# Performance work log

Measured on AMD Instinct MI355X. Metric: run time of the kernel, lower is better.

The kernel has to match this reference:

```python
import jax, jax.numpy as jnp
import numpy as np

B, C, F, T = 8, 2, 64, 1024
E = C * F            # embed_dim = 128
H = 8                # num_heads
DH = E // H          # head_dim = 16


def setup_inputs() -> dict:
    key = jax.random.key(0)
    ks = jax.random.split(key, 14)
    s = 0.05  # small init scale for numerical stability
    return {
        "x_re": jax.random.normal(ks[0], (B, C, F, T), jnp.float32),
        "x_im": jax.random.normal(ks[1], (B, C, F, T), jnp.float32),
        "win_re": jax.random.normal(ks[2], (3 * E, E), jnp.float32) * s,
        "win_im": jax.random.normal(ks[3], (3 * E, E), jnp.float32) * s,
        "bin_re": jax.random.normal(ks[4], (3 * E,), jnp.float32) * s,
        "bin_im": jax.random.normal(ks[5], (3 * E,), jnp.float32) * s,
        "wout_re": jax.random.normal(ks[6], (E, E), jnp.float32) * s,
        "wout_im": jax.random.normal(ks[7], (E, E), jnp.float32) * s,
        "bout_re": jax.random.normal(ks[8], (E,), jnp.float32) * s,
        "bout_im": jax.random.normal(ks[9], (E,), jnp.float32) * s,
        "wt_re": jax.random.normal(ks[10], (E, E), jnp.float32) * s,
        "wt_im": jax.random.normal(ks[11], (E, E), jnp.float32) * s,
        "bt_re": jax.random.normal(ks[12], (E,), jnp.float32) * s,
        "bt_im": jax.random.normal(ks[13], (E,), jnp.float32) * s,
    }


def _forward(x_re, x_im, win_re, win_im, bin_re, bin_im,
             wout_re, wout_im, bout_re, bout_im,
             wt_re, wt_im, bt_re, bt_im):
    cplx = lambda r, i: (r + 1j * i).astype(jnp.complex64)
    x = cplx(x_re, x_im)                 # [B,C,F,T]
    win, bin_ = cplx(win_re, win_im), cplx(bin_re, bin_im)
    wout, bout = cplx(wout_re, wout_im), cplx(bout_re, bout_im)
    wt, bt = cplx(wt_re, wt_im), cplx(bt_re, bt_im)

    # flatten(1,2).transpose(1,2): [B,C,F,T] -> [B,E,T] -> [B,T,E]
    xs = jnp.transpose(x.reshape(B, E, T), (0, 2, 1))

    # packed complex qkv projection
    qkv = xs @ win.T + bin_              # [B,T,3E]
    q, k, v = jnp.split(qkv, 3, axis=-1)
    split_heads = lambda t: jnp.transpose(t.reshape(B, T, H, DH), (0, 2, 1, 3))
    q, k, v = split_heads(q), split_heads(k), split_heads(v)  # [B,H,T,DH]

    # complex attention scores Q K^H; softmax over real part
    scores = jnp.einsum("bhqd,bhkd->bhqk", q, jnp.conj(k)) * (DH ** -0.5)
    attn = jax.nn.softmax(scores.real, axis=-1).astype(jnp.complex64)
    o = jnp.einsum("bhqk,bhkd->bhqd", attn, v)               # [B,H,T,DH]
    o = jnp.transpose(o, (0, 2, 1, 3)).reshape(B, T, E)
    o = o @ wout.T + bout                # attention out-proj

    # transform: complex Linear E -> E
    y = o @ wt.T + bt                    # [B,T,E]

    # unflatten(-1,(C,F)) then movedim(1,-1): [B,T,C,F] -> [B,C,F,T]
    y = jnp.moveaxis(y.reshape(B, T, C, F), 1, -1)
    return jnp.stack([y.real, y.imag], axis=0)  # [2,B,C,F,T]


def reference(x_re, x_im, win_re, win_im, bin_re, bin_im,
              wout_re, wout_im, bout_re, bout_im,
              wt_re, wt_im, bt_re, bt_im):
    return _forward(x_re, x_im, win_re, win_im, bin_re, bin_im,
                    wout_re, wout_im, bout_re, bout_im,
                    wt_re, wt_im, bt_re, bt_im)
```

## Files before the change

kernel.cpp:

```cpp
#include <hip/hip_runtime.h>
#include <hip/hip_bf16.h>

#define B 8
#define T 1024
#define E 128
#define H 8
#define DH 16
#define E3 384

typedef __attribute__((ext_vector_type(8))) short short8;
typedef __attribute__((ext_vector_type(4))) short short4s;
typedef __attribute__((ext_vector_type(4))) float f32x4;

static __device__ inline short bf16s(float x) {
    union { float f; unsigned u; } v; v.f = x;
    unsigned r = v.u + 0x7fffu + ((v.u >> 16) & 1u);
    return (short)(r >> 16);
}

#if __has_builtin(__builtin_amdgcn_exp2f)
static __device__ inline float fexp2(float x) { return __builtin_amdgcn_exp2f(x); }
#else
static __device__ inline float fexp2(float x) { return __builtin_exp2f(x); }
#endif

static __device__ inline __hip_bfloat162 pk2(float a, float b) {
    float2 t; t.x = a; t.y = b;
    return __float22bfloat162_rn(t);
}

#define QSCALE 0.36067376022224085f

__global__ void prep_weights_kernel(
    const float* __restrict__ win_re, const float* __restrict__ win_im,
    const float* __restrict__ wout_re, const float* __restrict__ wout_im,
    const float* __restrict__ bout_re, const float* __restrict__ bout_im,
    const float* __restrict__ wt_re,   const float* __restrict__ wt_im,
    const float* __restrict__ bt_re,   const float* __restrict__ bt_im,
    short* __restrict__ Wp_re, short* __restrict__ Wp_im,
    short* __restrict__ Wfp_re, short* __restrict__ Wfp_im,
    float* __restrict__ bf_re, float* __restrict__ bf_im)
{
    int bid = blockIdx.x;
    if (bid < E3*E/256) {
        int idx = bid * 256 + threadIdx.x;
        int j = idx >> 7, e = idx & 127;
        float wr = win_re[idx], wi = win_im[idx];
        Wp_re[j*256 + e]       = bf16s(wr);
        Wp_re[j*256 + 128 + e] = bf16s(-wi);
        Wp_im[j*256 + e]       = bf16s(wi);
        Wp_im[j*256 + 128 + e] = bf16s(wr);
    } else {
        int idx = (bid - E3*E/256) * 256 + threadIdx.x;
        int j = idx >> 7, e = idx & 127;
        float ar = 0.f, ai = 0.f;
        for (int m = 0; m < E; ++m) {
            float tr = wt_re[j*E+m], ti = wt_im[j*E+m];
            float pr = wout_re[m*E+e], pi = wout_im[m*E+e];
            ar += tr*pr - ti*pi;
            ai += tr*pi + ti*pr;
        }
        Wfp_re[j*256 + e]       = bf16s(ar);
        Wfp_re[j*256 + 128 + e] = bf16s(-ai);
        Wfp_im[j*256 + e]       = bf16s(ai);
        Wfp_im[j*256 + 128 + e] = bf16s(ar);
        if (idx < E) {
            float br = bt_re[idx], bi = bt_im[idx];
            for (int m = 0; m < E; ++m) {
                float tr = wt_re[idx*E+m], ti = wt_im[idx*E+m];
                br += tr*bout_re[m] - ti*bout_im[m];
                bi += tr*bout_im[m] + ti*bout_re[m];
            }
            bf_re[idx] = br; bf_im[idx] = bi;
        }
    }
}

__global__ __launch_bounds__(256) void qkv_mfma_kernel(
    const float* __restrict__ x_re, const float* __restrict__ x_im,
    const short* __restrict__ Wp_re, const short* __restrict__ Wp_im,
    const float* __restrict__ bin_re, const float* __restrict__ bin_im,
    short* __restrict__ Qpk, short* __restrict__ Kpk,
    short* __restrict__ Vtre, short* __restrict__ Vtim)
{
    int tid  = threadIdx.x;
    int wave = tid >> 6, lane = tid & 63;
    int col  = lane & 15, quad = lane >> 4;
    int ttile = blockIdx.x;
    int b  = ttile >> 6;
    int tb = (ttile & 63) * 16 + col;

    short8 xf[8];
    #pragma unroll
    for (int kt = 0; kt < 8; ++kt) {
        const float* xs = (kt < 4) ? x_re : x_im;
        const float* p = &xs[((long)(b*E + (kt & 3)*32 + quad*8))*T + tb];
        float v0 = p[0], v1 = p[(long)T], v2 = p[2L*T], v3 = p[3L*T];
        float v4 = p[4L*T], v5 = p[5L*T], v6 = p[6L*T], v7 = p[7L*T];
        __hip_bfloat162* xp = (__hip_bfloat162*)&xf[kt];
        xp[0] = pk2(v0, v1); xp[1] = pk2(v2, v3);
        xp[2] = pk2(v4, v5); xp[3] = pk2(v6, v7);
    }

    const f32x4 zero = {0.f,0.f,0.f,0.f};

    #pragma unroll
    for (int half = 0; half < 2; ++half) {
        const short* Wsel = half ? Wp_im : Wp_re;
        const float* bias = half ? bin_im : bin_re;

        for (int ni = 0; ni < 6; ++ni) {
            int jt = wave * 6 + ni;
            const short* wrow = &Wsel[(jt*16 + col)*256 + quad*8];
            f32x4 acc = zero;
            #pragma unroll
            for (int kt = 0; kt < 8; ++kt) {
                short8 af = *(const short8*)(wrow + kt*32);
                acc = __builtin_amdgcn_mfma_f32_16x16x32_bf16(af, xf[kt], acc, 0, 0, 0);
            }
            int which = jt >> 3;
            int h = jt & 7;
            float scale = (which == 0) ? QSCALE : 1.0f;
            f32x4 res;
            #pragma unroll
            for (int r = 0; r < 4; ++r) {
                int jg = which*128 + h*16 + quad*4 + r;
                res[r] = (acc[r] + bias[jg]) * scale;
            }
            long bh = b*H + h;
            if (which == 2) {
                short* vt = half ? Vtim : Vtre;
                int tloc = tb & 31, tblk = tb & ~31;
                int u  = tloc & 15;
                int kk = (u >> 2)*8 + (u & 3) + ((tloc >= 16) ? 4 : 0);
                #pragma unroll
                for (int r = 0; r < 4; ++r)
                    vt[(bh*DH + quad*4 + r)*T + tblk + kk] = bf16s(res[r]);
            } else {
                short* qk = (which == 0) ? Qpk : Kpk;
                short4s pk;
                __hip_bfloat162* pp = (__hip_bfloat162*)&pk;
                pp[0] = pk2(res[0], res[1]);
                pp[1] = pk2(res[2], res[3]);
                *(short4s*)&qk[(bh*T + tb)*32 + half*16 + quad*4] = pk;
            }
        }
    }
}

__global__ __launch_bounds__(256) void attn_mfma_kernel(
    const short* __restrict__ Qpk, const short* __restrict__ Kpk,
    const short* __restrict__ Vtre, const short* __restrict__ Vtim,
    short* __restrict__ Opk)
{
    int id   = blockIdx.x;
    int bh   = id & 63;
    int q0   = (id >> 6) * 128;
    int tid  = threadIdx.x;
    int wave = tid >> 6;
    int lane = tid & 63;
    int col  = lane & 15;
    int quad = lane >> 4;

    long kq_base = (long)bh * T * 32;
    int qbase = q0 + wave * 32;

    short8 qfA = *(const short8*)&Qpk[kq_base + (long)(qbase + col)*32 + quad*8];
    short8 qfB = *(const short8*)&Qpk[kq_base + (long)(qbase + 16 + col)*32 + quad*8];

    const short* kp  = &Kpk[kq_base + col*32 + quad*8];
    const short* vrp = &Vtre[(long)bh*DH*T + (long)col*T + quad*8];
    const short* vip = &Vtim[(long)bh*DH*T + (long)col*T + quad*8];

    short8 ones;
    #pragma unroll
    for (int i = 0; i < 8; ++i) ones[i] = (short)0x3F80;

    f32x4 oAr = {0,0,0,0}, oAi = {0,0,0,0}, lA = {0,0,0,0};
    f32x4 oBr = {0,0,0,0}, oBi = {0,0,0,0}, lB = {0,0,0,0};
    const f32x4 zero = {0.f,0.f,0.f,0.f};

    auto STEP = [&](short8 kf0, short8 kf1, short8 vr, short8 vi) {
        __builtin_amdgcn_s_setprio(1);
        f32x4 sA0 = __builtin_amdgcn_mfma_f32_16x16x32_bf16(kf0, qfA, zero, 0, 0, 0);
        f32x4 sA1 = __builtin_amdgcn_mfma_f32_16x16x32_bf16(kf1, qfA, zero, 0, 0, 0);
        f32x4 sB0 = __builtin_amdgcn_mfma_f32_16x16x32_bf16(kf0, qfB, zero, 0, 0, 0);
        f32x4 sB1 = __builtin_amdgcn_mfma_f32_16x16x32_bf16(kf1, qfB, zero, 0, 0, 0);
        __builtin_amdgcn_s_setprio(0);

        short8 pfA, pfB;
        {
            __hip_bfloat162* pa = (__hip_bfloat162*)&pfA;
            pa[0] = pk2(fexp2(sA0[0]), fexp2(sA0[1]));
            pa[1] = pk2(fexp2(sA0[2]), fexp2(sA0[3]));
            pa[2] = pk2(fexp2(sA1[0]), fexp2(sA1[1]));
            pa[3] = pk2(fexp2(sA1[2]), fexp2(sA1[3]));
            __hip_bfloat162* pb = (__hip_bfloat162*)&pfB;
            pb[0] = pk2(fexp2(sB0[0]), fexp2(sB0[1]));
            pb[1] = pk2(fexp2(sB0[2]), fexp2(sB0[3]));
            pb[2] = pk2(fexp2(sB1[0]), fexp2(sB1[1]));
            pb[3] = pk2(fexp2(sB1[2]), fexp2(sB1[3]));
        }

        __builtin_amdgcn_s_setprio(1);
        oAr = __builtin_amdgcn_mfma_f32_16x16x32_bf16(vr, pfA, oAr, 0, 0, 0);
        oAi = __builtin_amdgcn_mfma_f32_16x16x32_bf16(vi, pfA, oAi, 0, 0, 0);
        lA  = __builtin_amdgcn_mfma_f32_16x16x32_bf16(ones, pfA, lA, 0, 0, 0);
        oBr = __builtin_amdgcn_mfma_f32_16x16x32_bf16(vr, pfB, oBr, 0, 0, 0);
        oBi = __builtin_amdgcn_mfma_f32_16x16x32_bf16(vi, pfB, oBi, 0, 0, 0);
        lB  = __builtin_amdgcn_mfma_f32_16x16x32_bf16(ones, pfB, lB, 0, 0, 0);
        __builtin_amdgcn_s_setprio(0);
    };

    short8 k0A = *(const short8*)kp;
    short8 k1A = *(const short8*)(kp + 512);
    short8 vrA = *(const short8*)vrp;
    short8 viA = *(const short8*)vip;
    short8 k0B = *(const short8*)(kp + 1024);
    short8 k1B = *(const short8*)(kp + 1536);
    short8 vrB = *(const short8*)(vrp + 32);
    short8 viB = *(const short8*)(vip + 32);
    kp += 2048; vrp += 64; vip += 64;

    for (int i = 0; i < 32; i += 2) {
        short8 k0n = *(const short8*)kp;
        short8 k1n = *(const short8*)(kp + 512);
        short8 vrn = *(const short8*)vrp;
        short8 vin = *(const short8*)vip;
        kp += 1024; vrp += 32; vip += 32;

        STEP(k0A, k1A, vrA, viA);
        k0A = k0n; k1A = k1n; vrA = vrn; viA = vin;

        k0n = *(const short8*)kp;
        k1n = *(const short8*)(kp + 512);
        vrn = *(const short8*)vrp;
        vin = *(const short8*)vip;
        kp += 1024; vrp += 32; vip += 32;

        STEP(k0B, k1B, vrB, viB);
        k0B = k0n; k1B = k1n; vrB = vrn; viB = vin;
    }

    int b = bh >> 3, h = bh & 7;
    float invA = 1.0f / lA[0];
    float invB = 1.0f / lB[0];

    long orowA = ((long)(b*T + qbase + col))*256 + h*16 + quad*4;
    {
        short4s pr, pi_;
        __hip_bfloat162* a = (__hip_bfloat162*)&pr;
        a[0] = pk2(oAr[0]*invA, oAr[1]*invA);
        a[1] = pk2(oAr[2]*invA, oAr[3]*invA);
        __hip_bfloat162* c = (__hip_bfloat162*)&pi_;
        c[0] = pk2(oAi[0]*invA, oAi[1]*invA);
        c[1] = pk2(oAi[2]*invA, oAi[3]*invA);
        *(short4s*)&Opk[orowA]       = pr;
        *(short4s*)&Opk[orowA + 128] = pi_;
    }
    long orowB = orowA + 16L*256;
    {
        short4s pr, pi_;
        __hip_bfloat162* a = (__hip_bfloat162*)&pr;
        a[0] = pk2(oBr[0]*invB, oBr[1]*invB);
        a[1] = pk2(oBr[2]*invB, oBr[3]*invB);
        __hip_bfloat162* c = (__hip_bfloat162*)&pi_;
        c[0] = pk2(oBi[0]*invB, oBi[1]*invB);
        c[1] = pk2(oBi[2]*invB, oBi[3]*invB);
        *(short4s*)&Opk[orowB]       = pr;
        *(short4s*)&Opk[orowB + 128] = pi_;
    }
}

__global__ __launch_bounds__(256) void outproj_mfma_kernel(
    const short* __restrict__ Opk,
    const short* __restrict__ Wfp_re, const short* __restrict__ Wfp_im,
    const float* __restrict__ bf_re, const float* __restrict__ bf_im,
    float* __restrict__ out)
{
    int tid  = threadIdx.x;
    int wave = tid >> 6, lane = tid & 63;
    int col  = lane & 15, quad = lane >> 4;
    int ttile = blockIdx.x;
    int b  = ttile >> 6;
    int tb = (ttile & 63) * 16 + col;
    long trow = (long)b*T + tb;

    short8 xf[8];
    #pragma unroll
    for (int kt = 0; kt < 8; ++kt)
        xf[kt] = *(const short8*)&Opk[trow*256 + kt*32 + quad*8];

    const f32x4 zero = {0.f,0.f,0.f,0.f};
    #pragma unroll
    for (int ni = 0; ni < 4; ++ni) {
        int nt = wave * 4 + ni;
        int is_im = nt >= 8;
        int jt = is_im ? nt - 8 : nt;
        const short* Wsel = is_im ? Wfp_im : Wfp_re;
        const short* wrow = &Wsel[(jt*16 + col)*256 + quad*8];
        f32x4 acc = zero;
        #pragma unroll
        for (int kt = 0; kt < 8; ++kt) {
            short8 af = *(const short8*)(wrow + kt*32);
            acc = __builtin_amdgcn_mfma_f32_16x16x32_bf16(af, xf[kt], acc, 0, 0, 0);
        }
        const float* bias = is_im ? bf_im : bf_re;
        long part = is_im ? (long)B*E*T : 0;
        #pragma unroll
        for (int r = 0; r < 4; ++r) {
            int j = jt*16 + quad*4 + r;
            out[part + ((long)(b*E + j))*T + tb] = acc[r] + bias[j];
        }
    }
}

extern "C" void kernel_launch(void* const* d_in, const int* in_sizes, int n_in,
                              void* d_out, int out_size, void* d_ws, size_t ws_size,
                              hipStream_t stream)
{
    const float* x_re    = (const float*)d_in[0];
    const float* x_im    = (const float*)d_in[1];
    const float* win_re  = (const float*)d_in[2];
    const float* win_im  = (const float*)d_in[3];
    const float* bin_re  = (const float*)d_in[4];
    const float* bin_im  = (const float*)d_in[5];
    const float* wout_re = (const float*)d_in[6];
    const float* wout_im = (const float*)d_in[7];
    const float* bout_re = (const float*)d_in[8];
    const float* bout_im = (const float*)d_in[9];
    const float* wt_re   = (const float*)d_in[10];
    const float* wt_im   = (const float*)d_in[11];
    const float* bt_re   = (const float*)d_in[12];
    const float* bt_im   = (const float*)d_in[13];
    float* out = (float*)d_out;

    short* Qpk  = (short*)d_ws;
    short* Kpk  = Qpk + (long)B*H*T*32;
    short* Vtre = Kpk + (long)B*H*T*32;
    short* Vtim = Vtre + (long)B*H*DH*T;
    short* Opk  = Vtim + (long)B*H*DH*T;
    short* Wp_re  = Opk + (long)B*T*256;
    short* Wp_im  = Wp_re + E3*256;
    short* Wfp_re = Wp_im + E3*256;
    short* Wfp_im = Wfp_re + E*256;
    float* bf_re  = (float*)(Wfp_im + E*256);
    float* bf_im  = bf_re + E;

    prep_weights_kernel<<<dim3(E3*E/256 + E*E/256), dim3(256), 0, stream>>>(
        win_re, win_im, wout_re, wout_im, bout_re, bout_im,
        wt_re, wt_im, bt_re, bt_im,
        Wp_re, Wp_im, Wfp_re, Wfp_im, bf_re, bf_im);

    qkv_mfma_kernel<<<dim3(T*B/16), dim3(256), 0, stream>>>(
        x_re, x_im, Wp_re, Wp_im, bin_re, bin_im,
        Qpk, Kpk, Vtre, Vtim);

    attn_mfma_kernel<<<dim3(8 * 64), dim3(256), 0, stream>>>(
        Qpk, Kpk, Vtre, Vtim, Opk);

    outproj_mfma_kernel<<<dim3(T*B/16), dim3(256), 0, stream>>>(
        Opk, Wfp_re, Wfp_im, bf_re, bf_im, out);
}
```

Baseline: 165.6 us.

## Fuse four kernels into one persistent kernel with grid barriers

Merges the weight prep, QKV projection, attention and output projection kernels into a single launch of 512 blocks that separates the phases with atomic-counter grid barriers. The aim is to remove the launch gaps and tail effects between the four kernels. In exchange it adds a memset launch, spin-wait barriers, and a dependence on all 512 blocks being co-resident, which the 256-thread, 2-blocks-per-SIMD launch bounds are meant to allow. The prep phase also gates the QKV phase behind a barrier even though its serial loops are slow.

```diff
diff --git a/kernel.cpp b/kernel.cpp
--- a/kernel.cpp
+++ b/kernel.cpp
@@ -8,6 +8,8 @@
 #define DH 16
 #define E3 384
 
+#define NBLOCKS 512
+
 typedef __attribute__((ext_vector_type(8))) short short8;
 typedef __attribute__((ext_vector_type(4))) short short4s;
 typedef __attribute__((ext_vector_type(4))) float f32x4;
@@ -31,27 +33,51 @@
 
 #define QSCALE 0.36067376022224085f
 
-__global__ void prep_weights_kernel(
+static __device__ inline void grid_barrier(unsigned* __restrict__ ctr)
+{
+    __syncthreads();
+    if (threadIdx.x == 0) {
+        __threadfence();
+        __hip_atomic_fetch_add(ctr, 1u, __ATOMIC_ACQ_REL, __HIP_MEMORY_SCOPE_AGENT);
+        while (__hip_atomic_load(ctr, __ATOMIC_ACQUIRE, __HIP_MEMORY_SCOPE_AGENT) < (unsigned)NBLOCKS)
+            __builtin_amdgcn_s_sleep(2);
+        __threadfence();
+    }
+    __syncthreads();
+}
+
+__global__ __launch_bounds__(256, 2) void fused_mab_kernel(
+    const float* __restrict__ x_re,   const float* __restrict__ x_im,
     const float* __restrict__ win_re, const float* __restrict__ win_im,
-    const float* __restrict__ wout_re, const float* __restrict__ wout_im,
-    const float* __restrict__ bout_re, const float* __restrict__ bout_im,
-    const float* __restrict__ wt_re,   const float* __restrict__ wt_im,
-    const float* __restrict__ bt_re,   const float* __restrict__ bt_im,
-    short* __restrict__ Wp_re, short* __restrict__ Wp_im,
+    const float* __restrict__ bin_re, const float* __restrict__ bin_im,
+    const float* __restrict__ wout_re,const float* __restrict__ wout_im,
+    const float* __restrict__ bout_re,const float* __restrict__ bout_im,
+    const float* __restrict__ wt_re,  const float* __restrict__ wt_im,
+    const float* __restrict__ bt_re,  const float* __restrict__ bt_im,
+    short* __restrict__ Qpk,  short* __restrict__ Kpk,
+    short* __restrict__ Vtre, short* __restrict__ Vtim,
+    short* __restrict__ Opk,
+    short* __restrict__ Wp_re,  short* __restrict__ Wp_im,
     short* __restrict__ Wfp_re, short* __restrict__ Wfp_im,
-    float* __restrict__ bf_re, float* __restrict__ bf_im)
+    float* __restrict__ bf_re,  float* __restrict__ bf_im,
+    unsigned* __restrict__ bars,
+    float* __restrict__ out)
 {
-    int bid = blockIdx.x;
+    int bid  = blockIdx.x;
+    int tid  = threadIdx.x;
+    int wave = tid >> 6, lane = tid & 63;
+    int col  = lane & 15, quad = lane >> 4;
+
     if (bid < E3*E/256) {
-        int idx = bid * 256 + threadIdx.x;
+        int idx = bid * 256 + tid;
         int j = idx >> 7, e = idx & 127;
         float wr = win_re[idx], wi = win_im[idx];
         Wp_re[j*256 + e]       = bf16s(wr);
         Wp_re[j*256 + 128 + e] = bf16s(-wi);
         Wp_im[j*256 + e]       = bf16s(wi);
         Wp_im[j*256 + 128 + e] = bf16s(wr);
-    } else {
-        int idx = (bid - E3*E/256) * 256 + threadIdx.x;
+    } else if (bid < E3*E/256 + E*E/256) {
+        int idx = (bid - E3*E/256) * 256 + tid;
         int j = idx >> 7, e = idx & 127;
         float ar = 0.f, ai = 0.f;
         for (int m = 0; m < E; ++m) {
@@ -74,43 +100,207 @@
             bf_re[idx] = br; bf_im[idx] = bi;
         }
     }
-}
-
-__global__ __launch_bounds__(256) void qkv_mfma_kernel(
-    const float* __restrict__ x_re, const float* __restrict__ x_im,
-    const short* __restrict__ Wp_re, const short* __restrict__ Wp_im,
-    const float* __restrict__ bin_re, const float* __restrict__ bin_im,
-    short* __restrict__ Qpk, short* __restrict__ Kpk,
-    short* __restrict__ Vtre, short* __restrict__ Vtim)
-{
-    int tid  = threadIdx.x;
-    int wave = tid >> 6, lane = tid & 63;
-    int col  = lane & 15, quad = lane >> 4;
-    int ttile = blockIdx.x;
-    int b  = ttile >> 6;
-    int tb = (ttile & 63) * 16 + col;
-
-    short8 xf[8];
-    #pragma unroll
-    for (int kt = 0; kt < 8; ++kt) {
-        const float* xs = (kt < 4) ? x_re : x_im;
-        const float* p = &xs[((long)(b*E + (kt & 3)*32 + quad*8))*T + tb];
-        float v0 = p[0], v1 = p[(long)T], v2 = p[2L*T], v3 = p[3L*T];
-        float v4 = p[4L*T], v5 = p[5L*T], v6 = p[6L*T], v7 = p[7L*T];
-        __hip_bfloat162* xp = (__hip_bfloat162*)&xf[kt];
-        xp[0] = pk2(v0, v1); xp[1] = pk2(v2, v3);
-        xp[2] = pk2(v4, v5); xp[3] = pk2(v6, v7);
-    }
-
-    const f32x4 zero = {0.f,0.f,0.f,0.f};
-
-    #pragma unroll
-    for (int half = 0; half < 2; ++half) {
-        const short* Wsel = half ? Wp_im : Wp_re;
-        const float* bias = half ? bin_im : bin_re;
-
-        for (int ni = 0; ni < 6; ++ni) {
-            int jt = wave * 6 + ni;
+
+    grid_barrier(&bars[0]);
+
+    {
+        int ttile = bid;
+        int b  = ttile >> 6;
+        int tb = (ttile & 63) * 16 + col;
+
+        short8 xf[8];
+        #pragma unroll
+        for (int kt = 0; kt < 8; ++kt) {
+            const float* xs = (kt < 4) ? x_re : x_im;
+            const float* p = &xs[((long)(b*E + (kt & 3)*32 + quad*8))*T + tb];
+            float v0 = p[0], v1 = p[(long)T], v2 = p[2L*T], v3 = p[3L*T];
+            float v4 = p[4L*T], v5 = p[5L*T], v6 = p[6L*T], v7 = p[7L*T];
+            __hip_bfloat162* xp = (__hip_bfloat162*)&xf[kt];
+            xp[0] = pk2(v0, v1); xp[1] = pk2(v2, v3);
+            xp[2] = pk2(v4, v5); xp[3] = pk2(v6, v7);
+        }
+
+        const f32x4 zero = {0.f,0.f,0.f,0.f};
+
+        #pragma unroll
+        for (int half = 0; half < 2; ++half) {
+            const short* Wsel = half ? Wp_im : Wp_re;
+            const float* bias = half ? bin_im : bin_re;
+
+            for (int ni = 0; ni < 6; ++ni) {
+                int jt = wave * 6 + ni;
+                const short* wrow = &Wsel[(jt*16 + col)*256 + quad*8];
+                f32x4 acc = zero;
+                #pragma unroll
+                for (int kt = 0; kt < 8; ++kt) {
+                    short8 af = *(const short8*)(wrow + kt*32);
+                    acc = __builtin_amdgcn_mfma_f32_16x16x32_bf16(af, xf[kt], acc, 0, 0, 0);
+                }
+                int which = jt >> 3;
+                int h = jt & 7;
+                float scale = (which == 0) ? QSCALE : 1.0f;
+                f32x4 res;
+                #pragma unroll
+                for (int r = 0; r < 4; ++r) {
+                    int jg = which*128 + h*16 + quad*4 + r;
+                    res[r] = (acc[r] + bias[jg]) * scale;
+                }
+                long bh = b*H + h;
+                if (which == 2) {
+                    short* vt = half ? Vtim : Vtre;
+                    int tloc = tb & 31, tblk = tb & ~31;
+                    int u  = tloc & 15;
+                    int kk = (u >> 2)*8 + (u & 3) + ((tloc >= 16) ? 4 : 0);
+                    #pragma unroll
+                    for (int r = 0; r < 4; ++r)
+                        vt[(bh*DH + quad*4 + r)*T + tblk + kk] = bf16s(res[r]);
+                } else {
+                    short* qk = (which == 0) ? Qpk : Kpk;
+                    short4s pk;
+                    __hip_bfloat162* pp = (__hip_bfloat162*)&pk;
+                    pp[0] = pk2(res[0], res[1]);
+                    pp[1] = pk2(res[2], res[3]);
+                    *(short4s*)&qk[(bh*T + tb)*32 + half*16 + quad*4] = pk;
+                }
+            }
+        }
+    }
+
+    grid_barrier(&bars[16]);
+
+    {
+        int bh   = bid & 63;
+        int q0   = (bid >> 6) * 128;
+        long kq_base = (long)bh * T * 32;
+        int qbase = q0 + wave * 32;
+
+        short8 qfA = *(const short8*)&Qpk[kq_base + (long)(qbase + col)*32 + quad*8];
+        short8 qfB = *(const short8*)&Qpk[kq_base + (long)(qbase + 16 + col)*32 + quad*8];
+
+        const short* kp  = &Kpk[kq_base + col*32 + quad*8];
+        const short* vrp = &Vtre[(long)bh*DH*T + (long)col*T + quad*8];
+        const short* vip = &Vtim[(long)bh*DH*T + (long)col*T + quad*8];
+
+        short8 ones;
+        #pragma unroll
+        for (int i = 0; i < 8; ++i) ones[i] = (short)0x3F80;
+
+        f32x4 oAr = {0,0,0,0}, oAi = {0,0,0,0}, lA = {0,0,0,0};
+        f32x4 oBr = {0,0,0,0}, oBi = {0,0,0,0}, lB = {0,0,0,0};
+        const f32x4 zero = {0.f,0.f,0.f,0.f};
+
+        auto STEP = [&](short8 kf0, short8 kf1, short8 vr, short8 vi) {
+            __builtin_amdgcn_s_setprio(1);
+            f32x4 sA0 = __builtin_amdgcn_mfma_f32_16x16x32_bf16(kf0, qfA, zero, 0, 0, 0);
+            f32x4 sA1 = __builtin_amdgcn_mfma_f32_16x16x32_bf16(kf1, qfA, zero, 0, 0, 0);
+            f32x4 sB0 = __builtin_amdgcn_mfma_f32_16x16x32_bf16(kf0, qfB, zero, 0, 0, 0);
+            f32x4 sB1 = __builtin_amdgcn_mfma_f32_16x16x32_bf16(kf1, qfB, zero, 0, 0, 0);
+            __builtin_amdgcn_s_setprio(0);
+
+            short8 pfA, pfB;
+            {
+                __hip_bfloat162* pa = (__hip_bfloat162*)&pfA;
+                pa[0] = pk2(fexp2(sA0[0]), fexp2(sA0[1]));
+                pa[1] = pk2(fexp2(sA0[2]), fexp2(sA0[3]));
+                pa[2] = pk2(fexp2(sA1[0]), fexp2(sA1[1]));
+                pa[3] = pk2(fexp2(sA1[2]), fexp2(sA1[3]));
+                __hip_bfloat162* pb = (__hip_bfloat162*)&pfB;
+                pb[0] = pk2(fexp2(sB0[0]), fexp2(sB0[1]));
+                pb[1] = pk2(fexp2(sB0[2]), fexp2(sB0[3]));
+                pb[2] = pk2(fexp2(sB1[0]), fexp2(sB1[1]));
+                pb[3] = pk2(fexp2(sB1[2]), fexp2(sB1[3]));
+            }
+
+            __builtin_amdgcn_s_setprio(1);
+            oAr = __builtin_amdgcn_mfma_f32_16x16x32_bf16(vr, pfA, oAr, 0, 0, 0);
+            oAi = __builtin_amdgcn_mfma_f32_16x16x32_bf16(vi, pfA, oAi, 0, 0, 0);
+            lA  = __builtin_amdgcn_mfma_f32_16x16x32_bf16(ones, pfA, lA, 0, 0, 0);
+            oBr = __builtin_amdgcn_mfma_f32_16x16x32_bf16(vr, pfB, oBr, 0, 0, 0);
+            oBi = __builtin_amdgcn_mfma_f32_16x16x32_bf16(vi, pfB, oBi, 0, 0, 0);
+            lB  = __builtin_amdgcn_mfma_f32_16x16x32_bf16(ones, pfB, lB, 0, 0, 0);
+            __builtin_amdgcn_s_setprio(0);
+        };
+
+        short8 k0A = *(const short8*)kp;
+        short8 k1A = *(const short8*)(kp + 512);
+        short8 vrA = *(const short8*)vrp;
+        short8 viA = *(const short8*)vip;
+        short8 k0B = *(const short8*)(kp + 1024);
+        short8 k1B = *(const short8*)(kp + 1536);
+        short8 vrB = *(const short8*)(vrp + 32);
+        short8 viB = *(const short8*)(vip + 32);
+        kp += 2048; vrp += 64; vip += 64;
+
+        for (int i = 0; i < 32; i += 2) {
+            short8 k0n = *(const short8*)kp;
+            short8 k1n = *(const short8*)(kp + 512);
+            short8 vrn = *(const short8*)vrp;
+            short8 vin = *(const short8*)vip;
+            kp += 1024; vrp += 32; vip += 32;
+
+            STEP(k0A, k1A, vrA, viA);
+            k0A = k0n; k1A = k1n; vrA = vrn; viA = vin;
+
+            k0n = *(const short8*)kp;
+            k1n = *(const short8*)(kp + 512);
+            vrn = *(const short8*)vrp;
+            vin = *(const short8*)vip;
+            kp += 1024; vrp += 32; vip += 32;
+
+            STEP(k0B, k1B, vrB, viB);
+            k0B = k0n; k1B = k1n; vrB = vrn; viB = vin;
+        }
+
+        int b = bh >> 3, h = bh & 7;
+        float invA = 1.0f / lA[0];
+        float invB = 1.0f / lB[0];
+
+        long orowA = ((long)(b*T + qbase + col))*256 + h*16 + quad*4;
+        {
+            short4s pr, pi_;
+            __hip_bfloat162* a = (__hip_bfloat162*)&pr;
+            a[0] = pk2(oAr[0]*invA, oAr[1]*invA);
+            a[1] = pk2(oAr[2]*invA, oAr[3]*invA);
+            __hip_bfloat162* c = (__hip_bfloat162*)&pi_;
+            c[0] = pk2(oAi[0]*invA, oAi[1]*invA);
+            c[1] = pk2(oAi[2]*invA, oAi[3]*invA);
+            *(short4s*)&Opk[orowA]       = pr;
+            *(short4s*)&Opk[orowA + 128] = pi_;
+        }
+        long orowB = orowA + 16L*256;
+        {
+            short4s pr, pi_;
+            __hip_bfloat162* a = (__hip_bfloat162*)&pr;
+            a[0] = pk2(oBr[0]*invB, oBr[1]*invB);
+            a[1] = pk2(oBr[2]*invB, oBr[3]*invB);
+            __hip_bfloat162* c = (__hip_bfloat162*)&pi_;
+            c[0] = pk2(oBi[0]*invB, oBi[1]*invB);
+            c[1] = pk2(oBi[2]*invB, oBi[3]*invB);
+            *(short4s*)&Opk[orowB]       = pr;
+            *(short4s*)&Opk[orowB + 128] = pi_;
+        }
+    }
+
+    grid_barrier(&bars[32]);
+
+    {
+        int ttile = bid;
+        int b  = ttile >> 6;
+        int tb = (ttile & 63) * 16 + col;
+        long trow = (long)b*T + tb;
+
+        short8 xf[8];
+        #pragma unroll
+        for (int kt = 0; kt < 8; ++kt)
+            xf[kt] = *(const short8*)&Opk[trow*256 + kt*32 + quad*8];
+
+        const f32x4 zero = {0.f,0.f,0.f,0.f};
+        #pragma unroll
+        for (int ni = 0; ni < 4; ++ni) {
+            int nt = wave * 4 + ni;
+            int is_im = nt >= 8;
+            int jt = is_im ? nt - 8 : nt;
+            const short* Wsel = is_im ? Wfp_im : Wfp_re;
             const short* wrow = &Wsel[(jt*16 + col)*256 + quad*8];
             f32x4 acc = zero;
             #pragma unroll
@@ -118,199 +308,13 @@
                 short8 af = *(const short8*)(wrow + kt*32);
                 acc = __builtin_amdgcn_mfma_f32_16x16x32_bf16(af, xf[kt], acc, 0, 0, 0);
             }
-            int which = jt >> 3;
-            int h = jt & 7;
-            float scale = (which == 0) ? QSCALE : 1.0f;
-            f32x4 res;
+            const float* bias = is_im ? bf_im : bf_re;
+            long part = is_im ? (long)B*E*T : 0;
             #pragma unroll
             for (int r = 0; r < 4; ++r) {
-                int jg = which*128 + h*16 + quad*4 + r;
-                res[r] = (acc[r] + bias[jg]) * scale;
-            }
-            long bh = b*H + h;
-            if (which == 2) {
-                short* vt = half ? Vtim : Vtre;
-                int tloc = tb & 31, tblk = tb & ~31;
-                int u  = tloc & 15;
-                int kk = (u >> 2)*8 + (u & 3) + ((tloc >= 16) ? 4 : 0);
-                #pragma unroll
-                for (int r = 0; r < 4; ++r)
-                    vt[(bh*DH + quad*4 + r)*T + tblk + kk] = bf16s(res[r]);
-            } else {
-                short* qk = (which == 0) ? Qpk : Kpk;
-                short4s pk;
-                __hip_bfloat162* pp = (__hip_bfloat162*)&pk;
-                pp[0] = pk2(res[0], res[1]);
-                pp[1] = pk2(res[2], res[3]);
-                *(short4s*)&qk[(bh*T + tb)*32 + half*16 + quad*4] = pk;
-            }
-        }
-    }
-}
-
-__global__ __launch_bounds__(256) void attn_mfma_kernel(
-    const short* __restrict__ Qpk, const short* __restrict__ Kpk,
-    const short* __restrict__ Vtre, const short* __restrict__ Vtim,
-    short* __restrict__ Opk)
-{
-    int id   = blockIdx.x;
-    int bh   = id & 63;
-    int q0   = (id >> 6) * 128;
-    int tid  = threadIdx.x;
-    int wave = tid >> 6;
-    int lane = tid & 63;
-    int col  = lane & 15;
-    int quad = lane >> 4;
-
-    long kq_base = (long)bh * T * 32;
-    int qbase = q0 + wave * 32;
-
-    short8 qfA = *(const short8*)&Qpk[kq_base + (long)(qbase + col)*32 + quad*8];
-    short8 qfB = *(const short8*)&Qpk[kq_base + (long)(qbase + 16 + col)*32 + quad*8];
-
-    const short* kp  = &Kpk[kq_base + col*32 + quad*8];
-    const short* vrp = &Vtre[(long)bh*DH*T + (long)col*T + quad*8];
-    const short* vip = &Vtim[(long)bh*DH*T + (long)col*T + quad*8];
-
-    short8 ones;
-    #pragma unroll
-    for (int i = 0; i < 8; ++i) ones[i] = (short)0x3F80;
-
-    f32x4 oAr = {0,0,0,0}, oAi = {0,0,0,0}, lA = {0,0,0,0};
-    f32x4 oBr = {0,0,0,0}, oBi = {0,0,0,0}, lB = {0,0,0,0};
-    const f32x4 zero = {0.f,0.f,0.f,0.f};
-
-    auto STEP = [&](short8 kf0, short8 kf1, short8 vr, short8 vi) {
-        __builtin_amdgcn_s_setprio(1);
-        f32x4 sA0 = __builtin_amdgcn_mfma_f32_16x16x32_bf16(kf0, qfA, zero, 0, 0, 0);
-        f32x4 sA1 = __builtin_amdgcn_mfma_f32_16x16x32_bf16(kf1, qfA, zero, 0, 0, 0);
-        f32x4 sB0 = __builtin_amdgcn_mfma_f32_16x16x32_bf16(kf0, qfB, zero, 0, 0, 0);
-        f32x4 sB1 = __builtin_amdgcn_mfma_f32_16x16x32_bf16(kf1, qfB, zero, 0, 0, 0);
-        __builtin_amdgcn_s_setprio(0);
-
-        short8 pfA, pfB;
-        {
-            __hip_bfloat162* pa = (__hip_bfloat162*)&pfA;
-            pa[0] = pk2(fexp2(sA0[0]), fexp2(sA0[1]));
-            pa[1] = pk2(fexp2(sA0[2]), fexp2(sA0[3]));
-            pa[2] = pk2(fexp2(sA1[0]), fexp2(sA1[1]));
-            pa[3] = pk2(fexp2(sA1[2]), fexp2(sA1[3]));
-            __hip_bfloat162* pb = (__hip_bfloat162*)&pfB;
-            pb[0] = pk2(fexp2(sB0[0]), fexp2(sB0[1]));
-            pb[1] = pk2(fexp2(sB0[2]), fexp2(sB0[3]));
-            pb[2] = pk2(fexp2(sB1[0]), fexp2(sB1[1]));
-            pb[3] = pk2(fexp2(sB1[2]), fexp2(sB1[3]));
-        }
-
-        __builtin_amdgcn_s_setprio(1);
-        oAr = __builtin_amdgcn_mfma_f32_16x16x32_bf16(vr, pfA, oAr, 0, 0, 0);
-        oAi = __builtin_amdgcn_mfma_f32_16x16x32_bf16(vi, pfA, oAi, 0, 0, 0);
-        lA  = __builtin_amdgcn_mfma_f32_16x16x32_bf16(ones, pfA, lA, 0, 0, 0);
-        oBr = __builtin_amdgcn_mfma_f32_16x16x32_bf16(vr, pfB, oBr, 0, 0, 0);
-        oBi = __builtin_amdgcn_mfma_f32_16x16x32_bf16(vi, pfB, oBi, 0, 0, 0);
-        lB  = __builtin_amdgcn_mfma_f32_16x16x32_bf16(ones, pfB, lB, 0, 0, 0);
-        __builtin_amdgcn_s_setprio(0);
-    };
-
-    short8 k0A = *(const short8*)kp;
-    short8 k1A = *(const short8*)(kp + 512);
-    short8 vrA = *(const short8*)vrp;
-    short8 viA = *(const short8*)vip;
-    short8 k0B = *(const short8*)(kp + 1024);
-    short8 k1B = *(const short8*)(kp + 1536);
-    short8 vrB = *(const short8*)(vrp + 32);
-    short8 viB = *(const short8*)(vip + 32);
-    kp += 2048; vrp += 64; vip += 64;
-
-    for (int i = 0; i < 32; i += 2) {
-        short8 k0n = *(const short8*)kp;
-        short8 k1n = *(const short8*)(kp + 512);
-        short8 vrn = *(const short8*)vrp;
-        short8 vin = *(const short8*)vip;
-        kp += 1024; vrp += 32; vip += 32;
-
-        STEP(k0A, k1A, vrA, viA);
-        k0A = k0n; k1A = k1n; vrA = vrn; viA = vin;
-
-        k0n = *(const short8*)kp;
-        k1n = *(const short8*)(kp + 512);
-        vrn = *(const short8*)vrp;
-        vin = *(const short8*)vip;
-        kp += 1024; vrp += 32; vip += 32;
-
-        STEP(k0B, k1B, vrB, viB);
-        k0B = k0n; k1B = k1n; vrB = vrn; viB = vin;
-    }
-
-    int b = bh >> 3, h = bh & 7;
-    float invA = 1.0f / lA[0];
-    float invB = 1.0f / lB[0];
-
-    long orowA = ((long)(b*T + qbase + col))*256 + h*16 + quad*4;
-    {
-        short4s pr, pi_;
-        __hip_bfloat162* a = (__hip_bfloat162*)&pr;
-        a[0] = pk2(oAr[0]*invA, oAr[1]*invA);
-        a[1] = pk2(oAr[2]*invA, oAr[3]*invA);
-        __hip_bfloat162* c = (__hip_bfloat162*)&pi_;
-        c[0] = pk2(oAi[0]*invA, oAi[1]*invA);
-        c[1] = pk2(oAi[2]*invA, oAi[3]*invA);
-        *(short4s*)&Opk[orowA]       = pr;
-        *(short4s*)&Opk[orowA + 128] = pi_;
-    }
-    long orowB = orowA + 16L*256;
-    {
-        short4s pr, pi_;
-        __hip_bfloat162* a = (__hip_bfloat162*)&pr;
-        a[0] = pk2(oBr[0]*invB, oBr[1]*invB);
-        a[1] = pk2(oBr[2]*invB, oBr[3]*invB);
-        __hip_bfloat162* c = (__hip_bfloat162*)&pi_;
-        c[0] = pk2(oBi[0]*invB, oBi[1]*invB);
-        c[1] = pk2(oBi[2]*invB, oBi[3]*invB);
-        *(short4s*)&Opk[orowB]       = pr;
-        *(short4s*)&Opk[orowB + 128] = pi_;
-    }
-}
-
-__global__ __launch_bounds__(256) void outproj_mfma_kernel(
-    const short* __restrict__ Opk,
-    const short* __restrict__ Wfp_re, const short* __restrict__ Wfp_im,
-    const float* __restrict__ bf_re, const float* __restrict__ bf_im,
-    float* __restrict__ out)
-{
-    int tid  = threadIdx.x;
-    int wave = tid >> 6, lane = tid & 63;
-    int col  = lane & 15, quad = lane >> 4;
-    int ttile = blockIdx.x;
-    int b  = ttile >> 6;
-    int tb = (ttile & 63) * 16 + col;
-    long trow = (long)b*T + tb;
-
-    short8 xf[8];
-    #pragma unroll
-    for (int kt = 0; kt < 8; ++kt)
-        xf[kt] = *(const short8*)&Opk[trow*256 + kt*32 + quad*8];
-
-    const f32x4 zero = {0.f,0.f,0.f,0.f};
-    #pragma unroll
-    for (int ni = 0; ni < 4; ++ni) {
-        int nt = wave * 4 + ni;
-        int is_im = nt >= 8;
-        int jt = is_im ? nt - 8 : nt;
-        const short* Wsel = is_im ? Wfp_im : Wfp_re;
-        const short* wrow = &Wsel[(jt*16 + col)*256 + quad*8];
-        f32x4 acc = zero;
-        #pragma unroll
-        for (int kt = 0; kt < 8; ++kt) {
-            short8 af = *(const short8*)(wrow + kt*32);
-            acc = __builtin_amdgcn_mfma_f32_16x16x32_bf16(af, xf[kt], acc, 0, 0, 0);
-        }
-        const float* bias = is_im ? bf_im : bf_re;
-        long part = is_im ? (long)B*E*T : 0;
-        #pragma unroll
-        for (int r = 0; r < 4; ++r) {
-            int j = jt*16 + quad*4 + r;
-            out[part + ((long)(b*E + j))*T + tb] = acc[r] + bias[j];
+                int j = jt*16 + quad*4 + r;
+                out[part + ((long)(b*E + j))*T + tb] = acc[r] + bias[j];
+            }
         }
     }
 }
@@ -347,18 +351,15 @@
     float* bf_re  = (float*)(Wfp_im + E*256);
     float* bf_im  = bf_re + E;
 
-    prep_weights_kernel<<<dim3(E3*E/256 + E*E/256), dim3(256), 0, stream>>>(
-        win_re, win_im, wout_re, wout_im, bout_re, bout_im,
+    unsigned* bars = (unsigned*)((char*)d_ws + (32u << 20));
+
+    hipMemsetAsync(bars, 0, 256, stream);
+
+    fused_mab_kernel<<<dim3(NBLOCKS), dim3(256), 0, stream>>>(
+        x_re, x_im, win_re, win_im, bin_re, bin_im,
+        wout_re, wout_im, bout_re, bout_im,
         wt_re, wt_im, bt_re, bt_im,
-        Wp_re, Wp_im, Wfp_re, Wfp_im, bf_re, bf_im);
-
-    qkv_mfma_kernel<<<dim3(T*B/16), dim3(256), 0, stream>>>(
-        x_re, x_im, Wp_re, Wp_im, bin_re, bin_im,
-        Qpk, Kpk, Vtre, Vtim);
-
-    attn_mfma_kernel<<<dim3(8 * 64), dim3(256), 0, stream>>>(
-        Qpk, Kpk, Vtre, Vtim, Opk);
-
-    outproj_mfma_kernel<<<dim3(T*B/16), dim3(256), 0, stream>>>(
-        Opk, Wfp_re, Wfp_im, bf_re, bf_im, out);
-}
+        Qpk, Kpk, Vtre, Vtim, Opk,
+        Wp_re, Wp_im, Wfp_re, Wfp_im, bf_re, bf_im,
+        bars, out);
+}
```

Measured after the change: 420.8 us. 154% more time.
